# Kernel tuning notes

Measured on AMD Instinct MI355X. Metric: run time of the kernel, lower is better.

The kernel has to match this reference:

```python
import jax, jax.numpy as jnp
import numpy as np

B, T, D = 32, 2048, 512

def setup_inputs() -> dict:
    key = jax.random.key(0)
    x = jax.random.normal(key, (B, T, D), dtype=jnp.float32)
    return {"x": x}

def reference(x) -> jnp.ndarray:
    # w[b,t] = sum_s <x_bt, x_bs> - <x_bt, x_bt>
    # Equivalent to x_bt . (sum_s x_bs) - ||x_bt||^2; avoids the [B,T,T] matrix.
    s = x.sum(axis=1)                                  # [B, D]
    w = jnp.einsum('btd,bd->bt', x, s) - (x * x).sum(axis=-1)  # [B, T]
    weights = jax.nn.softmax(w, axis=1)                # softmax over time
    # weighted pooling over time -> [B, D]
    representations = jnp.einsum('btd,bt->bd', x, weights)
    return representations
```

## Files before the change

kernel.cpp:

```cpp
#include <hip/hip_runtime.h>
#include <math.h>

constexpr int B = 32;
constexpr int T = 2048;
constexpr int D = 512;

constexpr int C1 = 32;
constexpr int R1 = T / C1;
constexpr int C2 = 64;
constexpr int RW = 8;
constexpr int NPART = C2 * 4;

__global__ __launch_bounds__(256) void colsum_part(const float* __restrict__ x,
                                                   float* __restrict__ P1) {
    const int b = blockIdx.x, c = blockIdx.y;
    const int d4 = threadIdx.x & 127;
    const int rp = threadIdx.x >> 7;
    const float4* xp = (const float4*)x + ((size_t)(b * T + c * R1) * D >> 2)
                       + (size_t)rp * (D / 4) + d4;
    float4 acc = {0.f, 0.f, 0.f, 0.f};
    #pragma unroll 8
    for (int i = 0; i < R1 / 2; ++i) {
        float4 v = xp[(size_t)i * (D / 2)];
        acc.x += v.x; acc.y += v.y; acc.z += v.z; acc.w += v.w;
    }
    __shared__ float4 lds[128];
    if (rp == 1) lds[d4] = acc;
    __syncthreads();
    if (rp == 0) {
        float4 o = lds[d4];
        acc.x += o.x; acc.y += o.y; acc.z += o.z; acc.w += o.w;
        ((float4*)P1)[(size_t)(b * C1 + c) * (D / 4) + d4] = acc;
    }
}

__global__ __launch_bounds__(256) void reduce_s(const float* __restrict__ P1,
                                                float* __restrict__ s,
                                                float* __restrict__ out) {
    const int b = blockIdx.x;
    const int d4 = threadIdx.x & 127, half = threadIdx.x >> 7;
    const float4* pp = (const float4*)P1 + ((size_t)b * C1 + half * (C1 / 2)) * (D / 4) + d4;
    float4 acc = {0.f, 0.f, 0.f, 0.f};
    #pragma unroll
    for (int k = 0; k < C1 / 2; ++k) {
        float4 v = pp[(size_t)k * (D / 4)];
        acc.x += v.x; acc.y += v.y; acc.z += v.z; acc.w += v.w;
    }
    __shared__ float4 lds[128];
    if (half == 1) {
        lds[d4] = acc;
        ((float4*)out)[(size_t)b * (D / 4) + d4] = make_float4(0.f, 0.f, 0.f, 0.f);
    }
    __syncthreads();
    if (half == 0) {
        float4 o = lds[d4];
        acc.x += o.x; acc.y += o.y; acc.z += o.z; acc.w += o.w;
        ((float4*)s)[(size_t)b * (D / 4) + d4] = acc;
    }
}

__global__ __launch_bounds__(256) void fused_pool(const float* __restrict__ x,
                                                  const float* __restrict__ s,
                                                  float* __restrict__ Mp,
                                                  float* __restrict__ Sp,
                                                  float* __restrict__ Op) {
    const int b = blockIdx.x, c = blockIdx.y;
    const int wid = threadIdx.x >> 6, lane = threadIdx.x & 63;

    const float4* sp4 = (const float4*)(s + (size_t)b * D) + lane * 2;
    const float4 s0 = sp4[0], s1 = sp4[1];

    const int t0 = c * (RW * 4) + wid * RW;
    const float4* xr = (const float4*)(x + ((size_t)b * T + t0) * D) + lane * 2;

    float4 X0[RW], X1[RW];
    #pragma unroll
    for (int r = 0; r < RW; ++r) {
        X0[r] = xr[0]; X1[r] = xr[1];
        xr += D / 4;
    }
    float a[RW];
    #pragma unroll
    for (int r = 0; r < RW; ++r) {
        float t;
        t =      X0[r].x * (s0.x - X0[r].x);
        t = fmaf(X0[r].y,  s0.y - X0[r].y, t);
        t = fmaf(X0[r].z,  s0.z - X0[r].z, t);
        t = fmaf(X0[r].w,  s0.w - X0[r].w, t);
        t = fmaf(X1[r].x,  s1.x - X1[r].x, t);
        t = fmaf(X1[r].y,  s1.y - X1[r].y, t);
        t = fmaf(X1[r].z,  s1.z - X1[r].z, t);
        t = fmaf(X1[r].w,  s1.w - X1[r].w, t);
        a[r] = t;
    }

    #pragma unroll
    for (int off = 1; off < 64; off <<= 1) {
        #pragma unroll
        for (int r = 0; r < RW; ++r)
            a[r] += __shfl_xor(a[r], off, 64);
    }

    float m = fmaxf(fmaxf(fmaxf(a[0], a[1]), fmaxf(a[2], a[3])),
                    fmaxf(fmaxf(a[4], a[5]), fmaxf(a[6], a[7])));
    float e[RW], ssum = 0.f;
    #pragma unroll
    for (int r = 0; r < RW; ++r) { e[r] = __expf(a[r] - m); ssum += e[r]; }

    float4 O0 = {0.f,0.f,0.f,0.f}, O1 = {0.f,0.f,0.f,0.f};
    #pragma unroll
    for (int r = 0; r < RW; ++r) {
        O0.x = fmaf(e[r], X0[r].x, O0.x); O0.y = fmaf(e[r], X0[r].y, O0.y);
        O0.z = fmaf(e[r], X0[r].z, O0.z); O0.w = fmaf(e[r], X0[r].w, O0.w);
        O1.x = fmaf(e[r], X1[r].x, O1.x); O1.y = fmaf(e[r], X1[r].y, O1.y);
        O1.z = fmaf(e[r], X1[r].z, O1.z); O1.w = fmaf(e[r], X1[r].w, O1.w);
    }

    const int pi = (b * C2 + c) * 4 + wid;
    if (lane == 0) { Mp[pi] = m; Sp[pi] = ssum; }
    float4* op = (float4*)Op + (size_t)pi * (D / 4) + lane * 2;
    op[0] = O0; op[1] = O1;
}

__global__ __launch_bounds__(256) void merge_out(const float* __restrict__ Mp,
                                                 const float* __restrict__ Sp,
                                                 const float* __restrict__ Op,
                                                 float* __restrict__ out) {
    const int b = blockIdx.x, j = blockIdx.y;
    const int tid = threadIdx.x, wid = tid >> 6, lane = tid & 63;
    __shared__ float fsh[NPART];
    __shared__ float red[4];

    const float Mc = Mp[b * NPART + tid];
    float m = Mc;
    #pragma unroll
    for (int off = 1; off < 64; off <<= 1) m = fmaxf(m, __shfl_xor(m, off, 64));
    if (lane == 0) red[wid] = m;
    __syncthreads();
    const float Mg = fmaxf(fmaxf(red[0], red[1]), fmaxf(red[2], red[3]));
    __syncthreads();

    const float f = __expf(Mc - Mg);
    fsh[tid] = f;
    float spv = Sp[b * NPART + tid] * f;
    #pragma unroll
    for (int off = 1; off < 64; off <<= 1) spv += __shfl_xor(spv, off, 64);
    if (lane == 0) red[wid] = spv;
    __syncthreads();
    const float Sg = red[0] + red[1] + red[2] + red[3];
    const float inv = 1.0f / Sg;

    const int d4 = tid & 127, pr = tid >> 7;
    const int p0 = j * 32 + pr * 16;
    float4 acc = {0.f,0.f,0.f,0.f};
    const float4* op = (const float4*)Op + ((size_t)b * NPART + p0) * (D / 4) + d4;
    #pragma unroll 4
    for (int i = 0; i < 16; ++i) {
        const float fc = fsh[p0 + i];
        float4 v = op[(size_t)i * (D / 4)];
        acc.x = fmaf(fc, v.x, acc.x); acc.y = fmaf(fc, v.y, acc.y);
        acc.z = fmaf(fc, v.z, acc.z); acc.w = fmaf(fc, v.w, acc.w);
    }
    float* o = out + (size_t)b * D + d4 * 4;
    atomicAdd(o + 0, acc.x * inv);
    atomicAdd(o + 1, acc.y * inv);
    atomicAdd(o + 2, acc.z * inv);
    atomicAdd(o + 3, acc.w * inv);
}

extern "C" void kernel_launch(void* const* d_in, const int* in_sizes, int n_in,
                              void* d_out, int out_size, void* d_ws, size_t ws_size,
                              hipStream_t stream) {
    const float* x = (const float*)d_in[0];
    float* out = (float*)d_out;

    float* P1 = (float*)d_ws;
    float* s  = P1 + (size_t)B * C1 * D;
    float* Mp = s + (size_t)B * D;
    float* Sp = Mp + (size_t)B * NPART;
    float* Op = Sp + (size_t)B * NPART;

    colsum_part<<<dim3(B, C1), 256, 0, stream>>>(x, P1);
    reduce_s<<<B, 256, 0, stream>>>(P1, s, out);
    fused_pool<<<dim3(B, C2), 256, 0, stream>>>(x, s, Mp, Sp, Op);
    merge_out<<<dim3(B, 8), 256, 0, stream>>>(Mp, Sp, Op, out);
}
```

Baseline: 225.1 us.

## Fuse colsum reduction and merge into pool kernel via last-block counter

Cuts four kernel launches to two. Each pool block now reduces the 32 partial column sums into LDS itself, replacing the separate reduce_s kernel. Each block combines its four wave partials in LDS before writing one partial per block, and the last block per batch, found with an atomic counter, does the softmax merge and writes the output directly with no float atomics. The cost is redundant partial-sum loads (64 blocks per batch each read 64KB of P1), a serial merge tail in one block per batch, and fence and atomic overhead.

```diff
diff --git a/kernel.cpp b/kernel.cpp
--- a/kernel.cpp
+++ b/kernel.cpp
@@ -9,11 +9,12 @@
 constexpr int R1 = T / C1;
 constexpr int C2 = 64;
 constexpr int RW = 8;
-constexpr int NPART = C2 * 4;
 
 __global__ __launch_bounds__(256) void colsum_part(const float* __restrict__ x,
-                                                   float* __restrict__ P1) {
+                                                   float* __restrict__ P1,
+                                                   unsigned int* __restrict__ cnt) {
     const int b = blockIdx.x, c = blockIdx.y;
+    if (c == 0 && threadIdx.x == 0) cnt[b] = 0;
     const int d4 = threadIdx.x & 127;
     const int rp = threadIdx.x >> 7;
     const float4* xp = (const float4*)x + ((size_t)(b * T + c * R1) * D >> 2)
@@ -34,51 +35,43 @@
     }
 }
 
-__global__ __launch_bounds__(256) void reduce_s(const float* __restrict__ P1,
-                                                float* __restrict__ s,
-                                                float* __restrict__ out) {
-    const int b = blockIdx.x;
-    const int d4 = threadIdx.x & 127, half = threadIdx.x >> 7;
-    const float4* pp = (const float4*)P1 + ((size_t)b * C1 + half * (C1 / 2)) * (D / 4) + d4;
-    float4 acc = {0.f, 0.f, 0.f, 0.f};
-    #pragma unroll
-    for (int k = 0; k < C1 / 2; ++k) {
-        float4 v = pp[(size_t)k * (D / 4)];
-        acc.x += v.x; acc.y += v.y; acc.z += v.z; acc.w += v.w;
-    }
-    __shared__ float4 lds[128];
-    if (half == 1) {
-        lds[d4] = acc;
-        ((float4*)out)[(size_t)b * (D / 4) + d4] = make_float4(0.f, 0.f, 0.f, 0.f);
+__global__ __launch_bounds__(256) void fused_pool(const float* __restrict__ x,
+                                                  const float* __restrict__ P1,
+                                                  float* __restrict__ Mp,
+                                                  float* __restrict__ Sp,
+                                                  float* __restrict__ Op,
+                                                  unsigned int* __restrict__ cnt,
+                                                  float* __restrict__ out) {
+    const int b = blockIdx.x, c = blockIdx.y;
+    const int tid = threadIdx.x, wid = tid >> 6, lane = tid & 63;
+
+    __shared__ float  s_lds[D];
+    __shared__ float  mred[4], sred[4];
+    __shared__ float4 Obuf[4][D / 4];
+    __shared__ float  fmerge[C2];
+    __shared__ float  misc[2];
+    __shared__ int    lastflag;
+
+    {
+        const float2* pp = (const float2*)(P1 + (size_t)b * C1 * D) + tid;
+        float2 acc = {0.f, 0.f};
+        #pragma unroll
+        for (int k = 0; k < C1; ++k) {
+            float2 v = pp[(size_t)k * (D / 2)];
+            acc.x += v.x; acc.y += v.y;
+        }
+        ((float2*)s_lds)[tid] = acc;
     }
     __syncthreads();
-    if (half == 0) {
-        float4 o = lds[d4];
-        acc.x += o.x; acc.y += o.y; acc.z += o.z; acc.w += o.w;
-        ((float4*)s)[(size_t)b * (D / 4) + d4] = acc;
-    }
-}
+    const float4 s0 = ((const float4*)s_lds)[lane * 2];
+    const float4 s1 = ((const float4*)s_lds)[lane * 2 + 1];
 
-__global__ __launch_bounds__(256) void fused_pool(const float* __restrict__ x,
-                                                  const float* __restrict__ s,
-                                                  float* __restrict__ Mp,
-                                                  float* __restrict__ Sp,
-                                                  float* __restrict__ Op) {
-    const int b = blockIdx.x, c = blockIdx.y;
-    const int wid = threadIdx.x >> 6, lane = threadIdx.x & 63;
-
-    const float4* sp4 = (const float4*)(s + (size_t)b * D) + lane * 2;
-    const float4 s0 = sp4[0], s1 = sp4[1];
-
-    const int t0 = c * (RW * 4) + wid * RW;
+    const int t0 = c * (4 * RW) + wid * RW;
     const float4* xr = (const float4*)(x + ((size_t)b * T + t0) * D) + lane * 2;
-
     float4 X0[RW], X1[RW];
     #pragma unroll
-    for (int r = 0; r < RW; ++r) {
-        X0[r] = xr[0]; X1[r] = xr[1];
-        xr += D / 4;
-    }
+    for (int r = 0; r < RW; ++r) { X0[r] = xr[0]; X1[r] = xr[1]; xr += D / 4; }
+
     float a[RW];
     #pragma unroll
     for (int r = 0; r < RW; ++r) {
@@ -93,12 +86,10 @@
         t = fmaf(X1[r].w,  s1.w - X1[r].w, t);
         a[r] = t;
     }
-
     #pragma unroll
     for (int off = 1; off < 64; off <<= 1) {
         #pragma unroll
-        for (int r = 0; r < RW; ++r)
-            a[r] += __shfl_xor(a[r], off, 64);
+        for (int r = 0; r < RW; ++r) a[r] += __shfl_xor(a[r], off, 64);
     }
 
     float m = fmaxf(fmaxf(fmaxf(a[0], a[1]), fmaxf(a[2], a[3])),
@@ -116,56 +107,69 @@
         O1.z = fmaf(e[r], X1[r].z, O1.z); O1.w = fmaf(e[r], X1[r].w, O1.w);
     }
 
-    const int pi = (b * C2 + c) * 4 + wid;
-    if (lane == 0) { Mp[pi] = m; Sp[pi] = ssum; }
-    float4* op = (float4*)Op + (size_t)pi * (D / 4) + lane * 2;
-    op[0] = O0; op[1] = O1;
-}
+    if (lane == 0) { mred[wid] = m; sred[wid] = ssum; }
+    __syncthreads();
+    const float Mb = fmaxf(fmaxf(mred[0], mred[1]), fmaxf(mred[2], mred[3]));
+    const float fw = __expf(m - Mb);
+    float4 t0v = {O0.x * fw, O0.y * fw, O0.z * fw, O0.w * fw};
+    float4 t1v = {O1.x * fw, O1.y * fw, O1.z * fw, O1.w * fw};
+    Obuf[wid][lane * 2]     = t0v;
+    Obuf[wid][lane * 2 + 1] = t1v;
+    __syncthreads();
+    if (tid == 0) {
+        float Sb = sred[0] * __expf(mred[0] - Mb) + sred[1] * __expf(mred[1] - Mb)
+                 + sred[2] * __expf(mred[2] - Mb) + sred[3] * __expf(mred[3] - Mb);
+        Mp[b * C2 + c] = Mb;
+        Sp[b * C2 + c] = Sb;
+    }
+    if (tid < D / 4) {
+        float4 v0 = Obuf[0][tid], v1 = Obuf[1][tid], v2 = Obuf[2][tid], v3 = Obuf[3][tid];
+        float4 r;
+        r.x = (v0.x + v1.x) + (v2.x + v3.x);
+        r.y = (v0.y + v1.y) + (v2.y + v3.y);
+        r.z = (v0.z + v1.z) + (v2.z + v3.z);
+        r.w = (v0.w + v1.w) + (v2.w + v3.w);
+        ((float4*)Op)[(size_t)(b * C2 + c) * (D / 4) + tid] = r;
+    }
 
-__global__ __launch_bounds__(256) void merge_out(const float* __restrict__ Mp,
-                                                 const float* __restrict__ Sp,
-                                                 const float* __restrict__ Op,
-                                                 float* __restrict__ out) {
-    const int b = blockIdx.x, j = blockIdx.y;
-    const int tid = threadIdx.x, wid = tid >> 6, lane = tid & 63;
-    __shared__ float fsh[NPART];
-    __shared__ float red[4];
+    __threadfence();
+    __syncthreads();
+    if (tid == 0) {
+        unsigned int old = __hip_atomic_fetch_add(&cnt[b], 1u,
+                              __ATOMIC_ACQ_REL, __HIP_MEMORY_SCOPE_AGENT);
+        lastflag = (old == C2 - 1);
+    }
+    __syncthreads();
+    if (!lastflag) return;
+    __builtin_amdgcn_fence(__ATOMIC_ACQUIRE, "agent");
 
-    const float Mc = Mp[b * NPART + tid];
-    float m = Mc;
-    #pragma unroll
-    for (int off = 1; off < 64; off <<= 1) m = fmaxf(m, __shfl_xor(m, off, 64));
-    if (lane == 0) red[wid] = m;
+    if (wid == 0) {
+        const float Mc = Mp[b * C2 + lane];
+        float mm = Mc;
+        #pragma unroll
+        for (int off = 1; off < 64; off <<= 1) mm = fmaxf(mm, __shfl_xor(mm, off, 64));
+        const float fc = __expf(Mc - mm);
+        fmerge[lane] = fc;
+        float fs = fc * Sp[b * C2 + lane];
+        #pragma unroll
+        for (int off = 1; off < 64; off <<= 1) fs += __shfl_xor(fs, off, 64);
+        if (lane == 0) { misc[0] = mm; misc[1] = fs; }
+    }
     __syncthreads();
-    const float Mg = fmaxf(fmaxf(red[0], red[1]), fmaxf(red[2], red[3]));
-    __syncthreads();
-
-    const float f = __expf(Mc - Mg);
-    fsh[tid] = f;
-    float spv = Sp[b * NPART + tid] * f;
-    #pragma unroll
-    for (int off = 1; off < 64; off <<= 1) spv += __shfl_xor(spv, off, 64);
-    if (lane == 0) red[wid] = spv;
-    __syncthreads();
-    const float Sg = red[0] + red[1] + red[2] + red[3];
-    const float inv = 1.0f / Sg;
-
-    const int d4 = tid & 127, pr = tid >> 7;
-    const int p0 = j * 32 + pr * 16;
-    float4 acc = {0.f,0.f,0.f,0.f};
-    const float4* op = (const float4*)Op + ((size_t)b * NPART + p0) * (D / 4) + d4;
-    #pragma unroll 4
-    for (int i = 0; i < 16; ++i) {
-        const float fc = fsh[p0 + i];
-        float4 v = op[(size_t)i * (D / 4)];
-        acc.x = fmaf(fc, v.x, acc.x); acc.y = fmaf(fc, v.y, acc.y);
-        acc.z = fmaf(fc, v.z, acc.z); acc.w = fmaf(fc, v.w, acc.w);
+    const float invS = 1.0f / misc[1];
+    if (tid < D / 4) {
+        float4 acc = {0.f,0.f,0.f,0.f};
+        const float4* op = (const float4*)Op + (size_t)b * C2 * (D / 4) + tid;
+        #pragma unroll 4
+        for (int cc = 0; cc < C2; ++cc) {
+            const float fc = fmerge[cc];
+            float4 v = op[(size_t)cc * (D / 4)];
+            acc.x = fmaf(fc, v.x, acc.x); acc.y = fmaf(fc, v.y, acc.y);
+            acc.z = fmaf(fc, v.z, acc.z); acc.w = fmaf(fc, v.w, acc.w);
+        }
+        acc.x *= invS; acc.y *= invS; acc.z *= invS; acc.w *= invS;
+        ((float4*)out)[(size_t)b * (D / 4) + tid] = acc;
     }
-    float* o = out + (size_t)b * D + d4 * 4;
-    atomicAdd(o + 0, acc.x * inv);
-    atomicAdd(o + 1, acc.y * inv);
-    atomicAdd(o + 2, acc.z * inv);
-    atomicAdd(o + 3, acc.w * inv);
 }
 
 extern "C" void kernel_launch(void* const* d_in, const int* in_sizes, int n_in,
@@ -175,13 +179,11 @@
     float* out = (float*)d_out;
 
     float* P1 = (float*)d_ws;
-    float* s  = P1 + (size_t)B * C1 * D;
-    float* Mp = s + (size_t)B * D;
-    float* Sp = Mp + (size_t)B * NPART;
-    float* Op = Sp + (size_t)B * NPART;
+    float* Mp = P1 + (size_t)B * C1 * D;
+    float* Sp = Mp + (size_t)B * C2;
+    float* Op = Sp + (size_t)B * C2;
+    unsigned int* cnt = (unsigned int*)(Op + (size_t)B * C2 * D);
 
-    colsum_part<<<dim3(B, C1), 256, 0, stream>>>(x, P1);
-    reduce_s<<<B, 256, 0, stream>>>(P1, s, out);
-    fused_pool<<<dim3(B, C2), 256, 0, stream>>>(x, s, Mp, Sp, Op);
-    merge_out<<<dim3(B, 8), 256, 0, stream>>>(Mp, Sp, Op, out);
+    colsum_part<<<dim3(B, C1), 256, 0, stream>>>(x, P1, cnt);
+    fused_pool<<<dim3(B, C2), 256, 0, stream>>>(x, P1, Mp, Sp, Op, cnt, out);
 }
```

Result: slower. 499.1 us (+121.7%).
